# Performance work log

Hardware: AMD Instinct MI355X
Metric: run time of the kernel (lower is better)

The kernel has to match this reference:

```python
import jax, jax.numpy as jnp
import numpy as np

NUM_EXPERTS = 8
EXPERTS_PER_TOK = 2

def setup_inputs() -> dict:
    key = jax.random.key(0)
    k1, k2, k3, k4, k5 = jax.random.split(key, 5)
    B, T, D, F, E = 4, 1024, 2048, 1024, NUM_EXPERTS
    return {
        "x": jax.random.normal(k1, (B, T, D), dtype=jnp.float32),
        "router_w": jax.random.normal(k2, (D, E), dtype=jnp.float32) * 0.02,
        "gate_proj": jax.random.normal(k3, (E, D, F), dtype=jnp.float32) * 0.02,
        "up_proj": jax.random.normal(k4, (E, D, F), dtype=jnp.float32) * 0.02,
        "down_proj": jax.random.normal(k5, (E, F, D), dtype=jnp.float32) * 0.02,
    }

def reference(x, router_w, gate_proj, up_proj, down_proj):
    E, K = NUM_EXPERTS, EXPERTS_PER_TOK
    # Router: softmax over experts, take top-k, renormalize.
    scores = jnp.einsum('btd,de->bte', x, router_w).astype(jnp.float32)
    routing_weights, routing_idx = jax.lax.top_k(jax.nn.softmax(scores, axis=-1), K)
    routing_weights = (routing_weights / jnp.sum(routing_weights, axis=-1, keepdims=True)).astype(x.dtype)
    # one_hot: [B,T,K,E]. Sum over K gives 0/1 dispatch mask [B,T,E]
    # (top-k indices are distinct). Weighted sum gives combine weights.
    onehot = jax.nn.one_hot(routing_idx, E, dtype=x.dtype)
    dispatch_mask = jnp.sum(onehot, axis=2)                      # [B,T,E]
    combine_weights = jnp.einsum('btke,btk->bte', onehot, routing_weights)
    # Dense masked dispatch (same math as original einsum with size-1 I axis).
    dispatched = x[:, :, None, :] * dispatch_mask[..., None]     # [B,T,E,D]
    # SwiGLU FFN for every expert, batched over E.
    gate = jnp.einsum('bted,edf->btef', dispatched, gate_proj)
    up = jnp.einsum('bted,edf->btef', dispatched, up_proj)
    act = jax.nn.silu(gate) * up                                 # [B,T,E,F]
    expert_out = jnp.einsum('btef,efd->bted', act, down_proj)    # [B,T,E,D]
    # Combine: weights already include the dispatch mask via one-hot.
    return jnp.einsum('bted,bte->btd', expert_out, combine_weights)
```

## Files before the change

kernel.cpp:

```cpp
#include <hip/hip_runtime.h>
#include <stdint.h>

#define BT 4096
#define DMODEL 2048
#define FDIM 1024
#define NEXP 8
#define NA (BT * 2)
#define MAXT 40
#define NB1 (FDIM / 128)
#define NB2 (DMODEL / 256)
#define GRID1 (MAXT * NB1)
#define GRID2 (MAXT * NB2)
#define NT1 (DMODEL / 64)
#define NT2 (FDIM / 64)

typedef __attribute__((ext_vector_type(8))) __bf16 bf16x8;
typedef __attribute__((ext_vector_type(4))) float f32x4;

#define FENCE() asm volatile("" ::: "memory")
#define BARRIER() do { FENCE(); __builtin_amdgcn_s_barrier(); FENCE(); } while (0)
#define WAITVM0() asm volatile("s_waitcnt vmcnt(0)" ::: "memory")

__device__ __forceinline__ unsigned short f2bf(float f) {
  union { float f; unsigned int u; } v; v.f = f;
  unsigned int u = v.u;
  unsigned int r = (u + 0x7fffu + ((u >> 16) & 1u)) >> 16;
  return (unsigned short)r;
}
__device__ __forceinline__ float bf2f(unsigned short h) {
  union { unsigned int u; float f; } v; v.u = ((unsigned int)h) << 16;
  return v.f;
}

__device__ __forceinline__ void g2l16(const void* g, void* l) {
  __builtin_amdgcn_global_load_lds((const __attribute__((address_space(1))) void*)g,
                                   (__attribute__((address_space(3))) void*)l, 16, 0, 0);
}


__global__ void k_router(const float* __restrict__ x, const float* __restrict__ rw,
                         unsigned short* __restrict__ xbf,
                         int* __restrict__ tok_e, float* __restrict__ tok_w) {
  int wid = threadIdx.x >> 6;
  int lane = threadIdx.x & 63;
  int t = blockIdx.x * 4 + wid;
  float acc[8];
#pragma unroll
  for (int e = 0; e < 8; e++) acc[e] = 0.0f;
  const float* xr = x + (size_t)t * DMODEL;
  unsigned short* xbr = xbf + (size_t)t * DMODEL;
#pragma unroll
  for (int d0 = lane * 4; d0 < DMODEL; d0 += 256) {
    float4 xv = *(const float4*)(xr + d0);
    ushort4 o = make_ushort4(f2bf(xv.x), f2bf(xv.y), f2bf(xv.z), f2bf(xv.w));
    *(ushort4*)(xbr + d0) = o;
    const float* xs = &xv.x;
#pragma unroll
    for (int j = 0; j < 4; j++) {
      const float4* r4 = (const float4*)(rw + (size_t)(d0 + j) * NEXP);
      float4 ra = r4[0], rb = r4[1];
      float xj = xs[j];
      acc[0] += xj * ra.x; acc[1] += xj * ra.y; acc[2] += xj * ra.z; acc[3] += xj * ra.w;
      acc[4] += xj * rb.x; acc[5] += xj * rb.y; acc[6] += xj * rb.z; acc[7] += xj * rb.w;
    }
  }
#pragma unroll
  for (int e = 0; e < 8; e++) {
    float v = acc[e];
#pragma unroll
    for (int off = 32; off > 0; off >>= 1) v += __shfl_xor(v, off);
    acc[e] = v;
  }
  if (lane == 0) {
    int e0 = 0; float s0 = acc[0];
#pragma unroll
    for (int e = 1; e < 8; e++) if (acc[e] > s0) { s0 = acc[e]; e0 = e; }
    int e1 = (e0 == 0) ? 1 : 0; float s1 = acc[e1];
#pragma unroll
    for (int e = 0; e < 8; e++) if (e != e0 && acc[e] > s1) { s1 = acc[e]; e1 = e; }
    float w0 = 1.0f / (1.0f + __expf(s1 - s0));
    tok_e[t * 2] = e0; tok_e[t * 2 + 1] = e1;
    tok_w[t * 2] = w0; tok_w[t * 2 + 1] = 1.0f - w0;
  }
}

__global__ void k_scanbuild(const int* __restrict__ tok_e, int* __restrict__ offsets,
                            int* __restrict__ tile_e, int* __restrict__ tile_y,
                            int* __restrict__ ntiles, int* __restrict__ cursors) {
  __shared__ int hist[NEXP];
  int tid = threadIdx.x;
  if (tid < NEXP) hist[tid] = 0;
  __syncthreads();
  for (int i = tid; i < NA; i += 256) atomicAdd(&hist[tok_e[i]], 1);
  __syncthreads();
  if (tid == 0) {
    int s = 0;
    for (int e = 0; e < NEXP; e++) { offsets[e] = s; s += hist[e]; }
    offsets[NEXP] = s;
    int idx = 0;
    for (int e = 0; e < NEXP; e++) {
      int nt = (hist[e] + 255) >> 8;
      for (int y = 0; y < nt; y++) { tile_e[idx] = e; tile_y[idx] = y; idx++; }
    }
    *ntiles = idx;
    for (int i = idx; i < MAXT; i++) { tile_e[i] = 0; tile_y[i] = 0; }
  }
  if (tid < NEXP) cursors[tid] = 0;
}

__global__ void k_scatter(const int* __restrict__ tok_e, const float* __restrict__ tok_w,
                          const int* __restrict__ offsets, int* __restrict__ cursors,
                          int* __restrict__ assign_token, float* __restrict__ assign_w,
                          int* __restrict__ tok2pos) {
  int i = blockIdx.x * 256 + threadIdx.x;
  if (i >= NA) return;
  int e = tok_e[i];
  int pos = offsets[e] + atomicAdd(&cursors[e], 1);
  assign_token[pos] = i >> 1;
  assign_w[pos] = tok_w[i];
  tok2pos[i] = pos;
}

__global__ void k_transpose_all(const float* __restrict__ gw, const float* __restrict__ uw,
                                const float* __restrict__ dw,
                                unsigned short* __restrict__ wtg, unsigned short* __restrict__ wtu,
                                unsigned short* __restrict__ wtd) {
  __shared__ float tile[64][65];
  int z = blockIdx.y;
  const float* src; unsigned short* dst; int N;
  if (z < 8)       { src = gw + (size_t)z * DMODEL * FDIM;        dst = wtg + (size_t)z * DMODEL * FDIM;        N = FDIM; }
  else if (z < 16) { src = uw + (size_t)(z - 8) * DMODEL * FDIM;  dst = wtu + (size_t)(z - 8) * DMODEL * FDIM;  N = FDIM; }
  else             { src = dw + (size_t)(z - 16) * FDIM * DMODEL; dst = wtd + (size_t)(z - 16) * FDIM * DMODEL; N = DMODEL; }
  int ntx = N >> 6;
  int bx = blockIdx.x;
  int n0 = (bx % ntx) * 64, k0 = (bx / ntx) * 64;
  int rr = threadIdx.x >> 4, cc = threadIdx.x & 15;
#pragma unroll
  for (int i = 0; i < 4; i++) {
    int k = rr + i * 16;
    float4 v = *(const float4*)(src + (size_t)(k0 + k) * N + n0 + cc * 4);
    tile[k][cc * 4 + 0] = v.x; tile[k][cc * 4 + 1] = v.y;
    tile[k][cc * 4 + 2] = v.z; tile[k][cc * 4 + 3] = v.w;
  }
  __syncthreads();
  int K = (z < 16) ? DMODEL : FDIM;
#pragma unroll
  for (int i = 0; i < 4; i++) {
    int n = rr + i * 16;
    ushort4 o = make_ushort4(f2bf(tile[cc * 4 + 0][n]), f2bf(tile[cc * 4 + 1][n]),
                             f2bf(tile[cc * 4 + 2][n]), f2bf(tile[cc * 4 + 3][n]));
    *(ushort4*)(dst + (size_t)(n0 + n) * K + k0 + cc * 4) = o;
  }
}


__global__ __launch_bounds__(512, 2) void k_gemm1(
    const unsigned short* __restrict__ xbf,
    const unsigned short* __restrict__ wtg,
    const unsigned short* __restrict__ wtu,
    const int* __restrict__ offsets,
    const int* __restrict__ tile_e, const int* __restrict__ tile_y,
    const int* __restrict__ ntiles,
    const int* __restrict__ assign_token,
    unsigned short* __restrict__ act) {
  const int flat = blockIdx.x;
  const int wgid = (flat & 7) * (GRID1 / 8) + (flat >> 3);
  const int ti = wgid % MAXT;
  const int nb = wgid / MAXT;
  if (ti >= *ntiles) return;
  const int e = tile_e[ti];
  const int row_beg = offsets[e], row_end = offsets[e + 1];
  const int m_base = row_beg + tile_y[ti] * 256;
  const int n_base = nb * 128;

  __shared__ unsigned short As[2][256][64];
  __shared__ unsigned short Bg[2][128][64];
  __shared__ unsigned short Bu[2][128][64];

  const int tid = threadIdx.x;
  const int lane = tid & 63, wid = tid >> 6;
  const int wm = wid >> 2, wn = wid & 3;
  const int l15 = lane & 15;
  const int srow = tid >> 3;
  const int scol_d = (tid & 7) * 8;
  const int scol_s = ((tid & 7) ^ (srow & 7)) * 8;
  const int sw = (lane & 7) * 8;

  const unsigned short* wg_e = wtg + (size_t)e * FDIM * DMODEL + (size_t)n_base * DMODEL;
  const unsigned short* wu_e = wtu + (size_t)e * FDIM * DMODEL + (size_t)n_base * DMODEL;

  size_t arow[4];
#pragma unroll
  for (int i = 0; i < 4; i++) {
    int slot = m_base + i * 64 + srow;
    if (slot >= row_end) slot = row_end - 1;
    arow[i] = (size_t)assign_token[slot] * DMODEL;
  }

  f32x4 accg[8][2], accu[8][2];
#pragma unroll
  for (int m = 0; m < 8; m++)
#pragma unroll
    for (int n = 0; n < 2; n++) {
      accg[m][n] = f32x4{0.f, 0.f, 0.f, 0.f};
      accu[m][n] = f32x4{0.f, 0.f, 0.f, 0.f};
    }

  auto stageA = [&](int buf, int k0) {
#pragma unroll
    for (int i = 0; i < 4; i++)
      g2l16(xbf + arow[i] + k0 + scol_s, &As[buf][i * 64 + srow][scol_d]);
  };
  auto stageB = [&](int buf, int k0) {
#pragma unroll
    for (int i = 0; i < 2; i++)
      g2l16(wg_e + (size_t)(i * 64 + srow) * DMODEL + k0 + scol_s, &Bg[buf][i * 64 + srow][scol_d]);
#pragma unroll
    for (int i = 0; i < 2; i++)
      g2l16(wu_e + (size_t)(i * 64 + srow) * DMODEL + k0 + scol_s, &Bu[buf][i * 64 + srow][scol_d]);
  };

  stageA(0, 0); stageB(0, 0);
  WAITVM0(); BARRIER();

  for (int t = 0; t < NT1; ++t) {
    const int cur = t & 1, nxt = cur ^ 1;
    const int k1 = (t + 1) * 64;
    const bool pref = (t + 1 < NT1);

#pragma unroll
    for (int kk = 0; kk < 2; kk++) {
      const int ko = kk * 32 + (lane >> 4) * 8;
      bf16x8 a[8];
#pragma unroll
      for (int m = 0; m < 8; m++)
        a[m] = *(const bf16x8*)&As[cur][wm * 128 + m * 16 + l15][ko ^ sw];
      bf16x8 b0 = *(const bf16x8*)&Bg[cur][wn * 32 + l15][ko ^ sw];
      bf16x8 b1 = *(const bf16x8*)&Bg[cur][wn * 32 + 16 + l15][ko ^ sw];
      if (pref && kk == 0) stageA(nxt, k1);
      BARRIER();
      __builtin_amdgcn_s_setprio(1);
#pragma unroll
      for (int m = 0; m < 8; m++) {
        accg[m][0] = __builtin_amdgcn_mfma_f32_16x16x32_bf16(a[m], b0, accg[m][0], 0, 0, 0);
        accg[m][1] = __builtin_amdgcn_mfma_f32_16x16x32_bf16(a[m], b1, accg[m][1], 0, 0, 0);
      }
      __builtin_amdgcn_s_setprio(0);
      BARRIER();
      b0 = *(const bf16x8*)&Bu[cur][wn * 32 + l15][ko ^ sw];
      b1 = *(const bf16x8*)&Bu[cur][wn * 32 + 16 + l15][ko ^ sw];
      if (pref && kk == 0) stageB(nxt, k1);
      BARRIER();
      __builtin_amdgcn_s_setprio(1);
#pragma unroll
      for (int m = 0; m < 8; m++) {
        accu[m][0] = __builtin_amdgcn_mfma_f32_16x16x32_bf16(a[m], b0, accu[m][0], 0, 0, 0);
        accu[m][1] = __builtin_amdgcn_mfma_f32_16x16x32_bf16(a[m], b1, accu[m][1], 0, 0, 0);
      }
      __builtin_amdgcn_s_setprio(0);
      if (kk == 1 && pref) WAITVM0();
      BARRIER();
    }
  }

  const int cr = (lane >> 4) * 4;
#pragma unroll
  for (int m = 0; m < 8; m++) {
#pragma unroll
    for (int j = 0; j < 4; j++) {
      int slot = m_base + wm * 128 + m * 16 + cr + j;
      if (slot < row_end) {
        unsigned short* dst = act + (size_t)slot * FDIM + n_base + wn * 32 + l15;
#pragma unroll
        for (int n = 0; n < 2; n++) {
          float g = accg[m][n][j], u = accu[m][n][j];
          float h = (g / (1.0f + __expf(-g))) * u;
          dst[n * 16] = f2bf(h);
        }
      }
    }
  }
}


__global__ __launch_bounds__(512, 2) void k_gemm2(
    const unsigned short* __restrict__ act,
    const unsigned short* __restrict__ wtd,
    const int* __restrict__ offsets,
    const int* __restrict__ tile_e, const int* __restrict__ tile_y,
    const int* __restrict__ ntiles,
    const float* __restrict__ assign_w,
    unsigned short* __restrict__ out_pa) {
  const int flat = blockIdx.x;
  const int wgid = (flat & 7) * (GRID2 / 8) + (flat >> 3);
  const int ti = wgid % MAXT;
  const int nb = wgid / MAXT;
  if (ti >= *ntiles) return;
  const int e = tile_e[ti];
  const int row_beg = offsets[e], row_end = offsets[e + 1];
  const int m_base = row_beg + tile_y[ti] * 256;
  const int n_base = nb * 256;

  __shared__ unsigned short As[2][256][64];
  __shared__ unsigned short Bs[2][256][64];

  const int tid = threadIdx.x;
  const int lane = tid & 63, wid = tid >> 6;
  const int wm = wid >> 2, wn = wid & 3;
  const int l15 = lane & 15;
  const int srow = tid >> 3;
  const int scol_d = (tid & 7) * 8;
  const int scol_s = ((tid & 7) ^ (srow & 7)) * 8;
  const int sw = (lane & 7) * 8;

  const unsigned short* wd_e = wtd + (size_t)e * DMODEL * FDIM + (size_t)n_base * FDIM;

  size_t arow[4];
#pragma unroll
  for (int i = 0; i < 4; i++) {
    int slot = m_base + i * 64 + srow;
    if (slot >= row_end) slot = row_end - 1;
    arow[i] = (size_t)slot * FDIM;
  }

  f32x4 acc[8][4];
#pragma unroll
  for (int m = 0; m < 8; m++)
#pragma unroll
    for (int n = 0; n < 4; n++) acc[m][n] = f32x4{0.f, 0.f, 0.f, 0.f};

  auto stageA = [&](int buf, int k0) {
#pragma unroll
    for (int i = 0; i < 4; i++)
      g2l16(act + arow[i] + k0 + scol_s, &As[buf][i * 64 + srow][scol_d]);
  };
  auto stageB = [&](int buf, int k0) {
#pragma unroll
    for (int i = 0; i < 4; i++)
      g2l16(wd_e + (size_t)(i * 64 + srow) * FDIM + k0 + scol_s, &Bs[buf][i * 64 + srow][scol_d]);
  };

  stageA(0, 0); stageB(0, 0);
  WAITVM0(); BARRIER();

  for (int t = 0; t < NT2; ++t) {
    const int cur = t & 1, nxt = cur ^ 1;
    const int k1 = (t + 1) * 64;
    const bool pref = (t + 1 < NT2);

#pragma unroll
    for (int kk = 0; kk < 2; kk++) {
      const int ko = kk * 32 + (lane >> 4) * 8;
      bf16x8 a[8];
#pragma unroll
      for (int m = 0; m < 8; m++)
        a[m] = *(const bf16x8*)&As[cur][wm * 128 + m * 16 + l15][ko ^ sw];
      bf16x8 b0 = *(const bf16x8*)&Bs[cur][wn * 64 + l15][ko ^ sw];
      bf16x8 b1 = *(const bf16x8*)&Bs[cur][wn * 64 + 16 + l15][ko ^ sw];
      if (pref && kk == 0) stageA(nxt, k1);
      BARRIER();
      __builtin_amdgcn_s_setprio(1);
#pragma unroll
      for (int m = 0; m < 8; m++) {
        acc[m][0] = __builtin_amdgcn_mfma_f32_16x16x32_bf16(a[m], b0, acc[m][0], 0, 0, 0);
        acc[m][1] = __builtin_amdgcn_mfma_f32_16x16x32_bf16(a[m], b1, acc[m][1], 0, 0, 0);
      }
      __builtin_amdgcn_s_setprio(0);
      BARRIER();
      b0 = *(const bf16x8*)&Bs[cur][wn * 64 + 32 + l15][ko ^ sw];
      b1 = *(const bf16x8*)&Bs[cur][wn * 64 + 48 + l15][ko ^ sw];
      if (pref && kk == 0) stageB(nxt, k1);
      BARRIER();
      __builtin_amdgcn_s_setprio(1);
#pragma unroll
      for (int m = 0; m < 8; m++) {
        acc[m][2] = __builtin_amdgcn_mfma_f32_16x16x32_bf16(a[m], b0, acc[m][2], 0, 0, 0);
        acc[m][3] = __builtin_amdgcn_mfma_f32_16x16x32_bf16(a[m], b1, acc[m][3], 0, 0, 0);
      }
      __builtin_amdgcn_s_setprio(0);
      if (kk == 1 && pref) WAITVM0();
      BARRIER();
    }
  }

  const int cr = (lane >> 4) * 4;
#pragma unroll
  for (int m = 0; m < 8; m++) {
#pragma unroll
    for (int j = 0; j < 4; j++) {
      int slot = m_base + wm * 128 + m * 16 + cr + j;
      if (slot < row_end) {
        float w = assign_w[slot];
        unsigned short* dst = out_pa + (size_t)slot * DMODEL + n_base + wn * 64 + l15;
#pragma unroll
        for (int n = 0; n < 4; n++)
          dst[n * 16] = f2bf(acc[m][n][j] * w);
      }
    }
  }
}

__global__ void k_combine(const unsigned short* __restrict__ out_pa,
                          const int* __restrict__ tok2pos,
                          float* __restrict__ out) {
  int t = blockIdx.x;
  int p0 = tok2pos[t * 2], p1 = tok2pos[t * 2 + 1];
  int c = threadIdx.x;
  const ushort4* a = (const ushort4*)(out_pa + (size_t)p0 * DMODEL + c * 8);
  const ushort4* b = (const ushort4*)(out_pa + (size_t)p1 * DMODEL + c * 8);
  ushort4 a0 = a[0], a1 = a[1], b0 = b[0], b1 = b[1];
  float* o = out + (size_t)t * DMODEL + c * 8;
  o[0] = bf2f(a0.x) + bf2f(b0.x);
  o[1] = bf2f(a0.y) + bf2f(b0.y);
  o[2] = bf2f(a0.z) + bf2f(b0.z);
  o[3] = bf2f(a0.w) + bf2f(b0.w);
  o[4] = bf2f(a1.x) + bf2f(b1.x);
  o[5] = bf2f(a1.y) + bf2f(b1.y);
  o[6] = bf2f(a1.z) + bf2f(b1.z);
  o[7] = bf2f(a1.w) + bf2f(b1.w);
}


extern "C" void kernel_launch(void* const* d_in, const int* in_sizes, int n_in,
                              void* d_out, int out_size, void* d_ws, size_t ws_size,
                              hipStream_t stream) {
  const float* x  = (const float*)d_in[0];
  const float* rw = (const float*)d_in[1];
  const float* gw = (const float*)d_in[2];
  const float* uw = (const float*)d_in[3];
  const float* dw = (const float*)d_in[4];
  float* out = (float*)d_out;

  char* ws = (char*)d_ws;
  size_t off = 0;
  auto alloc = [&](size_t bytes) {
    size_t o = off;
    off += (bytes + 255) & ~(size_t)255;
    return o;
  };
  unsigned short* xbf    = (unsigned short*)(ws + alloc((size_t)BT * DMODEL * 2));
  unsigned short* wtg    = (unsigned short*)(ws + alloc((size_t)NEXP * FDIM * DMODEL * 2));
  unsigned short* wtu    = (unsigned short*)(ws + alloc((size_t)NEXP * FDIM * DMODEL * 2));
  unsigned short* wtd    = (unsigned short*)(ws + alloc((size_t)NEXP * DMODEL * FDIM * 2));
  unsigned short* act    = (unsigned short*)(ws + alloc((size_t)NA * FDIM * 2));
  unsigned short* out_pa = (unsigned short*)(ws + alloc((size_t)NA * DMODEL * 2));
  int*   offsets = (int*)(ws + alloc((NEXP + 1) * 4));
  int*   cursors = (int*)(ws + alloc(NEXP * 4));
  int*   tok_e   = (int*)(ws + alloc(NA * 4));
  float* tok_w   = (float*)(ws + alloc(NA * 4));
  int*   assign_token = (int*)(ws + alloc(NA * 4));
  float* assign_w     = (float*)(ws + alloc(NA * 4));
  int*   tok2pos      = (int*)(ws + alloc(NA * 4));
  int*   tile_e       = (int*)(ws + alloc(MAXT * 4));
  int*   tile_y       = (int*)(ws + alloc(MAXT * 4));
  int*   ntiles       = (int*)(ws + alloc(4));
  if (off > ws_size) return;

  k_router<<<BT / 4, 256, 0, stream>>>(x, rw, xbf, tok_e, tok_w);
  k_scanbuild<<<1, 256, 0, stream>>>(tok_e, offsets, tile_e, tile_y, ntiles, cursors);
  k_scatter<<<NA / 256, 256, 0, stream>>>(tok_e, tok_w, offsets, cursors,
                                          assign_token, assign_w, tok2pos);
  k_transpose_all<<<dim3(512, 24), 256, 0, stream>>>(gw, uw, dw, wtg, wtu, wtd);
  k_gemm1<<<GRID1, 512, 0, stream>>>(xbf, wtg, wtu, offsets,
                                     tile_e, tile_y, ntiles, assign_token, act);
  k_gemm2<<<GRID2, 512, 0, stream>>>(act, wtd, offsets,
                                     tile_e, tile_y, ntiles, assign_w, out_pa);
  k_combine<<<BT, 256, 0, stream>>>(out_pa, tok2pos, out);
}
```

Measured before the change: 344.9 us.

## Interleave gate/up weights and use triple-buffered vmcnt pipeline in expert GEMMs

Gate and up projection weights are interleaved in 16-row groups into one buffer, so gemm1 does a single 128-wide B tile whose two halves are gate and up, and the SiLU·up pair comes out of one accumulator set. Both GEMMs move from double buffering with several barriers per k-step to a three-stage LDS ring with partial vmcnt waits and one barrier per step. Gemm2 narrows its N tile to 128 and both launch on a 2D grid without the XCD swizzle. This cuts barrier and wait stalls and register pressure, but uses more LDS, halves per-block work in gemm1 (more blocks, more A reloads) and loses the L2-locality block remapping.

```diff
diff --git a/kernel.cpp b/kernel.cpp
--- a/kernel.cpp
+++ b/kernel.cpp
@@ -7,19 +7,16 @@
 #define NEXP 8
 #define NA (BT * 2)
 #define MAXT 40
-#define NB1 (FDIM / 128)
-#define NB2 (DMODEL / 256)
-#define GRID1 (MAXT * NB1)
-#define GRID2 (MAXT * NB2)
-#define NT1 (DMODEL / 64)
-#define NT2 (FDIM / 64)
+#define NB 16
 
 typedef __attribute__((ext_vector_type(8))) __bf16 bf16x8;
 typedef __attribute__((ext_vector_type(4))) float f32x4;
 
 #define FENCE() asm volatile("" ::: "memory")
 #define BARRIER() do { FENCE(); __builtin_amdgcn_s_barrier(); FENCE(); } while (0)
-#define WAITVM0() asm volatile("s_waitcnt vmcnt(0)" ::: "memory")
+#define VMCNT12() asm volatile("s_waitcnt vmcnt(12)" ::: "memory")
+#define VMCNT6()  asm volatile("s_waitcnt vmcnt(6)" ::: "memory")
+#define VMCNT0()  asm volatile("s_waitcnt vmcnt(0)" ::: "memory")
 
 __device__ __forceinline__ unsigned short f2bf(float f) {
   union { float f; unsigned int u; } v; v.f = f;
@@ -123,14 +120,14 @@
 
 __global__ void k_transpose_all(const float* __restrict__ gw, const float* __restrict__ uw,
                                 const float* __restrict__ dw,
-                                unsigned short* __restrict__ wtg, unsigned short* __restrict__ wtu,
+                                unsigned short* __restrict__ wtgu,
                                 unsigned short* __restrict__ wtd) {
   __shared__ float tile[64][65];
   int z = blockIdx.y;
-  const float* src; unsigned short* dst; int N;
-  if (z < 8)       { src = gw + (size_t)z * DMODEL * FDIM;        dst = wtg + (size_t)z * DMODEL * FDIM;        N = FDIM; }
-  else if (z < 16) { src = uw + (size_t)(z - 8) * DMODEL * FDIM;  dst = wtu + (size_t)(z - 8) * DMODEL * FDIM;  N = FDIM; }
-  else             { src = dw + (size_t)(z - 16) * FDIM * DMODEL; dst = wtd + (size_t)(z - 16) * FDIM * DMODEL; N = DMODEL; }
+  const float* src; unsigned short* dst; int N, Kd;
+  if (z < 8)       { src = gw + (size_t)z * DMODEL * FDIM;        dst = wtgu + (size_t)z * 2 * FDIM * DMODEL;        N = FDIM;   Kd = DMODEL; }
+  else if (z < 16) { src = uw + (size_t)(z - 8) * DMODEL * FDIM;  dst = wtgu + (size_t)(z - 8) * 2 * FDIM * DMODEL;  N = FDIM;   Kd = DMODEL; }
+  else             { src = dw + (size_t)(z - 16) * FDIM * DMODEL; dst = wtd + (size_t)(z - 16) * FDIM * DMODEL;      N = DMODEL; Kd = FDIM; }
   int ntx = N >> 6;
   int bx = blockIdx.x;
   int n0 = (bx % ntx) * 64, k0 = (bx / ntx) * 64;
@@ -143,39 +140,38 @@
     tile[k][cc * 4 + 2] = v.z; tile[k][cc * 4 + 3] = v.w;
   }
   __syncthreads();
-  int K = (z < 16) ? DMODEL : FDIM;
 #pragma unroll
   for (int i = 0; i < 4; i++) {
     int n = rr + i * 16;
+    int gr = n0 + n;
+    int orow;
+    if (z < 8)       orow = ((gr & ~15) << 1) + (gr & 15);
+    else if (z < 16) orow = ((gr & ~15) << 1) + 16 + (gr & 15);
+    else             orow = gr;
     ushort4 o = make_ushort4(f2bf(tile[cc * 4 + 0][n]), f2bf(tile[cc * 4 + 1][n]),
                              f2bf(tile[cc * 4 + 2][n]), f2bf(tile[cc * 4 + 3][n]));
-    *(ushort4*)(dst + (size_t)(n0 + n) * K + k0 + cc * 4) = o;
+    *(ushort4*)(dst + (size_t)orow * Kd + k0 + cc * 4) = o;
   }
 }
 
 
 __global__ __launch_bounds__(512, 2) void k_gemm1(
     const unsigned short* __restrict__ xbf,
-    const unsigned short* __restrict__ wtg,
-    const unsigned short* __restrict__ wtu,
+    const unsigned short* __restrict__ wtgu,
     const int* __restrict__ offsets,
     const int* __restrict__ tile_e, const int* __restrict__ tile_y,
     const int* __restrict__ ntiles,
     const int* __restrict__ assign_token,
     unsigned short* __restrict__ act) {
-  const int flat = blockIdx.x;
-  const int wgid = (flat & 7) * (GRID1 / 8) + (flat >> 3);
-  const int ti = wgid % MAXT;
-  const int nb = wgid / MAXT;
+  const int ti = blockIdx.y;
   if (ti >= *ntiles) return;
   const int e = tile_e[ti];
   const int row_beg = offsets[e], row_end = offsets[e + 1];
   const int m_base = row_beg + tile_y[ti] * 256;
-  const int n_base = nb * 128;
-
-  __shared__ unsigned short As[2][256][64];
-  __shared__ unsigned short Bg[2][128][64];
-  __shared__ unsigned short Bu[2][128][64];
+  const int n_base = blockIdx.x * 128;
+
+  __shared__ unsigned short As[3][256][64];
+  __shared__ unsigned short Bs[3][128][64];
 
   const int tid = threadIdx.x;
   const int lane = tid & 63, wid = tid >> 6;
@@ -186,8 +182,7 @@
   const int scol_s = ((tid & 7) ^ (srow & 7)) * 8;
   const int sw = (lane & 7) * 8;
 
-  const unsigned short* wg_e = wtg + (size_t)e * FDIM * DMODEL + (size_t)n_base * DMODEL;
-  const unsigned short* wu_e = wtu + (size_t)e * FDIM * DMODEL + (size_t)n_base * DMODEL;
+  const unsigned short* wb = wtgu + (size_t)e * 2 * FDIM * DMODEL + (size_t)n_base * DMODEL;
 
   size_t arow[4];
 #pragma unroll
@@ -197,86 +192,64 @@
     arow[i] = (size_t)assign_token[slot] * DMODEL;
   }
 
-  f32x4 accg[8][2], accu[8][2];
+  f32x4 acc[8][2];
 #pragma unroll
   for (int m = 0; m < 8; m++)
 #pragma unroll
-    for (int n = 0; n < 2; n++) {
-      accg[m][n] = f32x4{0.f, 0.f, 0.f, 0.f};
-      accu[m][n] = f32x4{0.f, 0.f, 0.f, 0.f};
-    }
-
-  auto stageA = [&](int buf, int k0) {
+    for (int n = 0; n < 2; n++) acc[m][n] = f32x4{0.f, 0.f, 0.f, 0.f};
+
+  auto stage = [&](int buf, int t) {
+    const int k0 = t * 64;
 #pragma unroll
     for (int i = 0; i < 4; i++)
       g2l16(xbf + arow[i] + k0 + scol_s, &As[buf][i * 64 + srow][scol_d]);
+#pragma unroll
+    for (int i = 0; i < 2; i++)
+      g2l16(wb + (size_t)(i * 64 + srow) * DMODEL + k0 + scol_s, &Bs[buf][i * 64 + srow][scol_d]);
   };
-  auto stageB = [&](int buf, int k0) {
-#pragma unroll
-    for (int i = 0; i < 2; i++)
-      g2l16(wg_e + (size_t)(i * 64 + srow) * DMODEL + k0 + scol_s, &Bg[buf][i * 64 + srow][scol_d]);
-#pragma unroll
-    for (int i = 0; i < 2; i++)
-      g2l16(wu_e + (size_t)(i * 64 + srow) * DMODEL + k0 + scol_s, &Bu[buf][i * 64 + srow][scol_d]);
-  };
-
-  stageA(0, 0); stageB(0, 0);
-  WAITVM0(); BARRIER();
-
-  for (int t = 0; t < NT1; ++t) {
-    const int cur = t & 1, nxt = cur ^ 1;
-    const int k1 = (t + 1) * 64;
-    const bool pref = (t + 1 < NT1);
-
+
+  const int NT = DMODEL / 64;
+  stage(0, 0); stage(1, 1); stage(2, 2);
+
+  int cur = 0;
+  for (int t = 0; t < NT; ++t) {
+    const int rem = NT - 1 - t;
+    if (rem >= 2) { VMCNT12(); } else if (rem == 1) { VMCNT6(); } else { VMCNT0(); }
+    BARRIER();
 #pragma unroll
     for (int kk = 0; kk < 2; kk++) {
       const int ko = kk * 32 + (lane >> 4) * 8;
-      bf16x8 a[8];
+      bf16x8 a[8], b[2];
 #pragma unroll
       for (int m = 0; m < 8; m++)
         a[m] = *(const bf16x8*)&As[cur][wm * 128 + m * 16 + l15][ko ^ sw];
-      bf16x8 b0 = *(const bf16x8*)&Bg[cur][wn * 32 + l15][ko ^ sw];
-      bf16x8 b1 = *(const bf16x8*)&Bg[cur][wn * 32 + 16 + l15][ko ^ sw];
-      if (pref && kk == 0) stageA(nxt, k1);
-      BARRIER();
+#pragma unroll
+      for (int n = 0; n < 2; n++)
+        b[n] = *(const bf16x8*)&Bs[cur][wn * 32 + n * 16 + l15][ko ^ sw];
       __builtin_amdgcn_s_setprio(1);
 #pragma unroll
       for (int m = 0; m < 8; m++) {
-        accg[m][0] = __builtin_amdgcn_mfma_f32_16x16x32_bf16(a[m], b0, accg[m][0], 0, 0, 0);
-        accg[m][1] = __builtin_amdgcn_mfma_f32_16x16x32_bf16(a[m], b1, accg[m][1], 0, 0, 0);
+        acc[m][0] = __builtin_amdgcn_mfma_f32_16x16x32_bf16(a[m], b[0], acc[m][0], 0, 0, 0);
+        acc[m][1] = __builtin_amdgcn_mfma_f32_16x16x32_bf16(a[m], b[1], acc[m][1], 0, 0, 0);
       }
       __builtin_amdgcn_s_setprio(0);
-      BARRIER();
-      b0 = *(const bf16x8*)&Bu[cur][wn * 32 + l15][ko ^ sw];
-      b1 = *(const bf16x8*)&Bu[cur][wn * 32 + 16 + l15][ko ^ sw];
-      if (pref && kk == 0) stageB(nxt, k1);
-      BARRIER();
-      __builtin_amdgcn_s_setprio(1);
-#pragma unroll
-      for (int m = 0; m < 8; m++) {
-        accu[m][0] = __builtin_amdgcn_mfma_f32_16x16x32_bf16(a[m], b0, accu[m][0], 0, 0, 0);
-        accu[m][1] = __builtin_amdgcn_mfma_f32_16x16x32_bf16(a[m], b1, accu[m][1], 0, 0, 0);
-      }
-      __builtin_amdgcn_s_setprio(0);
-      if (kk == 1 && pref) WAITVM0();
-      BARRIER();
-    }
+    }
+    BARRIER();
+    if (t + 3 < NT) stage(cur, t + 3);
+    cur = (cur == 2) ? 0 : cur + 1;
   }
 
   const int cr = (lane >> 4) * 4;
+  const int fcol = ((n_base + wn * 32) >> 1) + l15;
 #pragma unroll
   for (int m = 0; m < 8; m++) {
 #pragma unroll
     for (int j = 0; j < 4; j++) {
       int slot = m_base + wm * 128 + m * 16 + cr + j;
       if (slot < row_end) {
-        unsigned short* dst = act + (size_t)slot * FDIM + n_base + wn * 32 + l15;
-#pragma unroll
-        for (int n = 0; n < 2; n++) {
-          float g = accg[m][n][j], u = accu[m][n][j];
-          float h = (g / (1.0f + __expf(-g))) * u;
-          dst[n * 16] = f2bf(h);
-        }
+        float g = acc[m][0][j], u = acc[m][1][j];
+        float h = (g / (1.0f + __expf(-g))) * u;
+        act[(size_t)slot * FDIM + fcol] = f2bf(h);
       }
     }
   }
@@ -291,18 +264,15 @@
     const int* __restrict__ ntiles,
     const float* __restrict__ assign_w,
     unsigned short* __restrict__ out_pa) {
-  const int flat = blockIdx.x;
-  const int wgid = (flat & 7) * (GRID2 / 8) + (flat >> 3);
-  const int ti = wgid % MAXT;
-  const int nb = wgid / MAXT;
+  const int ti = blockIdx.y;
   if (ti >= *ntiles) return;
   const int e = tile_e[ti];
   const int row_beg = offsets[e], row_end = offsets[e + 1];
   const int m_base = row_beg + tile_y[ti] * 256;
-  const int n_base = nb * 256;
-
-  __shared__ unsigned short As[2][256][64];
-  __shared__ unsigned short Bs[2][256][64];
+  const int n_base = blockIdx.x * 128;
+
+  __shared__ unsigned short As[3][256][64];
+  __shared__ unsigned short Bs[3][128][64];
 
   const int tid = threadIdx.x;
   const int lane = tid & 63, wid = tid >> 6;
@@ -323,64 +293,51 @@
     arow[i] = (size_t)slot * FDIM;
   }
 
-  f32x4 acc[8][4];
+  f32x4 acc[8][2];
 #pragma unroll
   for (int m = 0; m < 8; m++)
 #pragma unroll
-    for (int n = 0; n < 4; n++) acc[m][n] = f32x4{0.f, 0.f, 0.f, 0.f};
-
-  auto stageA = [&](int buf, int k0) {
+    for (int n = 0; n < 2; n++) acc[m][n] = f32x4{0.f, 0.f, 0.f, 0.f};
+
+  auto stage = [&](int buf, int t) {
+    const int k0 = t * 64;
 #pragma unroll
     for (int i = 0; i < 4; i++)
       g2l16(act + arow[i] + k0 + scol_s, &As[buf][i * 64 + srow][scol_d]);
-  };
-  auto stageB = [&](int buf, int k0) {
-#pragma unroll
-    for (int i = 0; i < 4; i++)
+#pragma unroll
+    for (int i = 0; i < 2; i++)
       g2l16(wd_e + (size_t)(i * 64 + srow) * FDIM + k0 + scol_s, &Bs[buf][i * 64 + srow][scol_d]);
   };
 
-  stageA(0, 0); stageB(0, 0);
-  WAITVM0(); BARRIER();
-
-  for (int t = 0; t < NT2; ++t) {
-    const int cur = t & 1, nxt = cur ^ 1;
-    const int k1 = (t + 1) * 64;
-    const bool pref = (t + 1 < NT2);
-
+  const int NT = FDIM / 64;
+  stage(0, 0); stage(1, 1); stage(2, 2);
+
+  int cur = 0;
+  for (int t = 0; t < NT; ++t) {
+    const int rem = NT - 1 - t;
+    if (rem >= 2) { VMCNT12(); } else if (rem == 1) { VMCNT6(); } else { VMCNT0(); }
+    BARRIER();
 #pragma unroll
     for (int kk = 0; kk < 2; kk++) {
       const int ko = kk * 32 + (lane >> 4) * 8;
-      bf16x8 a[8];
+      bf16x8 a[8], b[2];
 #pragma unroll
       for (int m = 0; m < 8; m++)
         a[m] = *(const bf16x8*)&As[cur][wm * 128 + m * 16 + l15][ko ^ sw];
-      bf16x8 b0 = *(const bf16x8*)&Bs[cur][wn * 64 + l15][ko ^ sw];
-      bf16x8 b1 = *(const bf16x8*)&Bs[cur][wn * 64 + 16 + l15][ko ^ sw];
-      if (pref && kk == 0) stageA(nxt, k1);
-      BARRIER();
+#pragma unroll
+      for (int n = 0; n < 2; n++)
+        b[n] = *(const bf16x8*)&Bs[cur][wn * 32 + n * 16 + l15][ko ^ sw];
       __builtin_amdgcn_s_setprio(1);
 #pragma unroll
       for (int m = 0; m < 8; m++) {
-        acc[m][0] = __builtin_amdgcn_mfma_f32_16x16x32_bf16(a[m], b0, acc[m][0], 0, 0, 0);
-        acc[m][1] = __builtin_amdgcn_mfma_f32_16x16x32_bf16(a[m], b1, acc[m][1], 0, 0, 0);
+        acc[m][0] = __builtin_amdgcn_mfma_f32_16x16x32_bf16(a[m], b[0], acc[m][0], 0, 0, 0);
+        acc[m][1] = __builtin_amdgcn_mfma_f32_16x16x32_bf16(a[m], b[1], acc[m][1], 0, 0, 0);
       }
       __builtin_amdgcn_s_setprio(0);
-      BARRIER();
-      b0 = *(const bf16x8*)&Bs[cur][wn * 64 + 32 + l15][ko ^ sw];
-      b1 = *(const bf16x8*)&Bs[cur][wn * 64 + 48 + l15][ko ^ sw];
-      if (pref && kk == 0) stageB(nxt, k1);
-      BARRIER();
-      __builtin_amdgcn_s_setprio(1);
-#pragma unroll
-      for (int m = 0; m < 8; m++) {
-        acc[m][2] = __builtin_amdgcn_mfma_f32_16x16x32_bf16(a[m], b0, acc[m][2], 0, 0, 0);
-        acc[m][3] = __builtin_amdgcn_mfma_f32_16x16x32_bf16(a[m], b1, acc[m][3], 0, 0, 0);
-      }
-      __builtin_amdgcn_s_setprio(0);
-      if (kk == 1 && pref) WAITVM0();
-      BARRIER();
-    }
+    }
+    BARRIER();
+    if (t + 3 < NT) stage(cur, t + 3);
+    cur = (cur == 2) ? 0 : cur + 1;
   }
 
   const int cr = (lane >> 4) * 4;
@@ -391,9 +348,9 @@
       int slot = m_base + wm * 128 + m * 16 + cr + j;
       if (slot < row_end) {
         float w = assign_w[slot];
-        unsigned short* dst = out_pa + (size_t)slot * DMODEL + n_base + wn * 64 + l15;
-#pragma unroll
-        for (int n = 0; n < 4; n++)
+        unsigned short* dst = out_pa + (size_t)slot * DMODEL + n_base + wn * 32 + l15;
+#pragma unroll
+        for (int n = 0; n < 2; n++)
           dst[n * 16] = f2bf(acc[m][n][j] * w);
       }
     }
@@ -439,8 +396,7 @@
     return o;
   };
   unsigned short* xbf    = (unsigned short*)(ws + alloc((size_t)BT * DMODEL * 2));
-  unsigned short* wtg    = (unsigned short*)(ws + alloc((size_t)NEXP * FDIM * DMODEL * 2));
-  unsigned short* wtu    = (unsigned short*)(ws + alloc((size_t)NEXP * FDIM * DMODEL * 2));
+  unsigned short* wtgu   = (unsigned short*)(ws + alloc((size_t)NEXP * 2 * FDIM * DMODEL * 2));
   unsigned short* wtd    = (unsigned short*)(ws + alloc((size_t)NEXP * DMODEL * FDIM * 2));
   unsigned short* act    = (unsigned short*)(ws + alloc((size_t)NA * FDIM * 2));
   unsigned short* out_pa = (unsigned short*)(ws + alloc((size_t)NA * DMODEL * 2));
@@ -460,10 +416,12 @@
   k_scanbuild<<<1, 256, 0, stream>>>(tok_e, offsets, tile_e, tile_y, ntiles, cursors);
   k_scatter<<<NA / 256, 256, 0, stream>>>(tok_e, tok_w, offsets, cursors,
                                           assign_token, assign_w, tok2pos);
-  k_transpose_all<<<dim3(512, 24), 256, 0, stream>>>(gw, uw, dw, wtg, wtu, wtd);
-  k_gemm1<<<GRID1, 512, 0, stream>>>(xbf, wtg, wtu, offsets,
-                                     tile_e, tile_y, ntiles, assign_token, act);
-  k_gemm2<<<GRID2, 512, 0, stream>>>(act, wtd, offsets,
-                                     tile_e, tile_y, ntiles, assign_w, out_pa);
+  k_transpose_all<<<dim3(512, 24), 256, 0, stream>>>(gw, uw, dw, wtgu, wtd);
+  k_gemm1<<<dim3(NB, MAXT), 512, 0, stream>>>(xbf, wtgu, offsets,
+                                              tile_e, tile_y, ntiles,
+                                              assign_token, act);
+  k_gemm2<<<dim3(NB, MAXT), 512, 0, stream>>>(act, wtd, offsets,
+                                              tile_e, tile_y, ntiles,
+                                              assign_w, out_pa);
   k_combine<<<BT, 256, 0, stream>>>(out_pa, tok2pos, out);
 }
```

After: 380.3 us. 1.1x slower.
